# Optimization experiments

Hardware: AMD Instinct MI355X
Metric: run time of the kernel (lower is better)

Reference implementation:

```python
import jax, jax.numpy as jnp
import numpy as np

NUM_SEG = 533  # ~ 400*400/300 superpixels from SLIC
C_FEAT = 2112
H = W = 400
SIM_THRESH = 0.97


def setup_inputs() -> dict:
    key = jax.random.key(0)
    ks = jax.random.split(key, 8)
    inp = {
        "feature_maps": jax.random.normal(ks[0], (C_FEAT, H, W), jnp.float32),
        "sp": jax.random.randint(ks[1], (H, W), 0, NUM_SEG, jnp.int32),
        "y": jax.random.randint(ks[2], (H, W), 0, 3, jnp.int32),
        "w1": jax.random.normal(ks[3], (C_FEAT, 1024), jnp.float32) * 0.02,
        "b1": jnp.zeros((1024,), jnp.float32),
        "w2": jax.random.normal(ks[4], (1024, 1024), jnp.float32) * 0.02,
        "b2": jnp.zeros((1024,), jnp.float32),
        "w3": jax.random.normal(ks[5], (1024, 32), jnp.float32) * 0.02,
        "b3": jnp.zeros((32,), jnp.float32),
        "wc": jax.random.normal(ks[6], (32, 2), jnp.float32) * 0.02,
        "bc": jnp.zeros((2,), jnp.float32),
    }
    return inp


def reference(feature_maps, sp, y, w1, b1, w2, b2, w3, b3, wc, bc):
    C = feature_maps.shape[0]
    feats = feature_maps.reshape(C, -1).T            # [HW, C]
    seg = sp.reshape(-1)                             # [HW]

    # fused per-superpixel gather + mean (replaces the per-segment Python loop)
    sums = jax.ops.segment_sum(feats, seg, num_segments=NUM_SEG)          # [S, C]
    cnts = jax.ops.segment_sum(jnp.ones_like(seg, dtype=feats.dtype), seg,
                               num_segments=NUM_SEG)                      # [S]
    mean_feat = sums / jnp.maximum(cnts, 1.0)[:, None]                    # [S, C]

    # per-superpixel majority label over classes {0,1,2}
    onehot = jax.nn.one_hot(y.reshape(-1), 3, dtype=jnp.float32)          # [HW, 3]
    counts = jax.ops.segment_sum(onehot, seg, num_segments=NUM_SEG)       # [S, 3]
    lab = jnp.argmax(counts, axis=1)                                      # first max, like torch
    ones_c, twos_c = counts[:, 1], counts[:, 2]
    tie_break = jnp.where(twos_c > ones_c, 2, jnp.where(ones_c > twos_c, 1, 0))
    lab = jnp.where(lab == 0, tie_break, lab)                             # [S]

    # batched MLP + classifier (replaces per-segment calls)
    h = jax.nn.relu(mean_feat @ w1 + b1)
    h = jax.nn.relu(h @ w2 + b2)
    h = jax.nn.relu(h @ w3 + b3)
    preds = jax.nn.softmax(h @ wc + bc, axis=-1)                          # [S, 2]

    # cosine-similarity kNN label propagation (matmul form of the O(n*m) loop)
    labeled = lab != 0
    det = jax.lax.stop_gradient(mean_feat)
    nrm = det / jnp.maximum(jnp.linalg.norm(det, axis=1, keepdims=True), 1e-12)
    aff = nrm @ nrm.T                                                     # [S, S]
    aff_masked = jnp.where(labeled[None, :], aff, -jnp.inf)               # cols: labeled only
    best = jnp.max(aff_masked, axis=1)
    best_idx = jnp.argmax(aff_masked, axis=1)
    propagate = (~labeled) & (best >= SIM_THRESH)
    new_lab = jnp.where(propagate, lab[best_idx], lab)                    # [S]

    return preds, lab, labeled, new_lab
```

## Files before the change

kernel.cpp:

```cpp
#include <hip/hip_runtime.h>
#include <math.h>

#define NSEG 533
#define CFEAT 2112
#define PIX 160000
#define SIM_THRESH 0.97f
#define RPG 1250
#define NCG 33
#define RTOT (RPG * NCG)
#define NBLK 256

typedef __attribute__((ext_vector_type(4))) float f32x4;
typedef __attribute__((ext_vector_type(4))) int   i32x4;
typedef __attribute__((ext_vector_type(8))) short bf16x8;

__device__ inline unsigned short f2bf_u16(float f) {
    unsigned u = __builtin_bit_cast(unsigned, f);
    return (unsigned short)((u + 0x7FFFu + ((u >> 16) & 1u)) >> 16);
}
__device__ inline unsigned pkbf(float a, float b) {
    unsigned r;
    asm("v_cvt_pk_bf16_f32 %0, %1, %2" : "=v"(r) : "v"(a), "v"(b));
    return r;
}

__global__ __launch_bounds__(256) void k_counts(const int* __restrict__ sp,
                                                const int* __restrict__ y,
                                                int* __restrict__ c3) {
    int p = blockIdx.x * 256 + threadIdx.x;
    if (p < PIX) atomicAdd(&c3[sp[p] * 3 + y[p]], 1);
}

__global__ __launch_bounds__(256) void k_labels(const int* __restrict__ c3,
                                                int* __restrict__ lab,
                                                float* __restrict__ invc,
                                                float* __restrict__ out) {
    int s = blockIdx.x * 256 + threadIdx.x;
    if (s >= NSEG) return;
    int c0 = c3[s * 3 + 0], c1 = c3[s * 3 + 1], c2 = c3[s * 3 + 2];
    int cnt = c0 + c1 + c2;
    int idx = 0, best = c0;
    if (c1 > best) { best = c1; idx = 1; }
    if (c2 > best) { best = c2; idx = 2; }
    if (idx == 0) idx = (c2 > c1) ? 2 : ((c1 > c2) ? 1 : 0);
    lab[s] = idx;
    invc[s] = 1.0f / (float)(cnt > 0 ? cnt : 1);
    out[1066 + s] = (float)idx;
    out[1599 + s] = (idx != 0) ? 1.0f : 0.0f;
}

__global__ __launch_bounds__(1024, 4) void k_segsum_mfma(const float* __restrict__ fm,
                                                         const int* __restrict__ sp,
                                                         float* __restrict__ sums) {
    __shared__ char Bs[2][64 * 256];
    const int tid = threadIdx.x;
    const int lane = tid & 63, wave = tid >> 6;
    const int r = lane & 15, kg = lane >> 4;
    const int nmt = (wave < 2) ? 3 : 2;
    const int rswz = (r & 7) << 4;
    const int sch = tid >> 4;
    const int spx = tid & 15;
    const int wswz = (sch & 7) << 4;

    long long t0 = ((long long)blockIdx.x * RTOT) / NBLK;
    const long long t1 = ((long long)(blockIdx.x + 1) * RTOT) / NBLK;

    while (t0 < t1) {
        const int cg = (int)(t0 / RPG);
        const int r0 = (int)(t0 - (long long)cg * RPG);
        const long long cgend = (long long)(cg + 1) * RPG;
        const int rend = (int)(((t1 < cgend) ? t1 : cgend) - (long long)cg * RPG);
        const int c0 = cg * 64;
        const float* fmg = fm + (size_t)(c0 + sch) * PIX;

        f32x4 acc[3][4] = {};

        {
            const float* src = fmg + r0 * 128 + spx * 8;
            f32x4 u0 = *(const f32x4*)src;
            f32x4 u1 = *(const f32x4*)(src + 4);
            uint4 w = { pkbf(u0[0], u0[1]), pkbf(u0[2], u0[3]),
                        pkbf(u1[0], u1[1]), pkbf(u1[2], u1[3]) };
            *(uint4*)(Bs[r0 & 1] + sch * 256 + ((spx * 16) ^ wswz)) = w;
        }
        __syncthreads();

        for (int rr = r0; rr < rend; ++rr) {
            const bool pf = (rr + 1 < rend);
            f32x4 u0 = {}, u1 = {};
            if (pf) {
                const float* src = fmg + (rr + 1) * 128 + spx * 8;
                u0 = *(const f32x4*)src;
                u1 = *(const f32x4*)(src + 4);
            }
            const char* bufc = Bs[rr & 1];
            const int* spr = sp + rr * 128 + kg * 8;
            i32x4 sa = *(const i32x4*)spr;
            i32x4 sb = *(const i32x4*)(spr + 4);

            #pragma unroll
            for (int ks = 0; ks < 4; ++ks) {
                i32x4 na, nb;
                if (ks < 3) {
                    na = *(const i32x4*)(spr + (ks + 1) * 32);
                    nb = *(const i32x4*)(spr + (ks + 1) * 32 + 4);
                }
                bf16x8 vb[4];
                #pragma unroll
                for (int nt = 0; nt < 4; ++nt) {
                    vb[nt] = *(const bf16x8*)(bufc + (nt * 16 + r) * 256 +
                                              ((ks * 64 + kg * 16) ^ rswz));
                }
                int seg[8] = { sa[0], sa[1], sa[2], sa[3], sb[0], sb[1], sb[2], sb[3] };
                #pragma unroll
                for (int i = 0; i < 3; ++i) {
                    if (i < nmt) {
                        const int tm = (i < 2) ? wave * 2 + i : 32 + wave;
                        const int tgt = tm * 16 + r;
                        unsigned w0 = ((seg[0] == tgt) ? 0x00003F80u : 0u) |
                                      ((seg[1] == tgt) ? 0x3F800000u : 0u);
                        unsigned w1 = ((seg[2] == tgt) ? 0x00003F80u : 0u) |
                                      ((seg[3] == tgt) ? 0x3F800000u : 0u);
                        unsigned w2 = ((seg[4] == tgt) ? 0x00003F80u : 0u) |
                                      ((seg[5] == tgt) ? 0x3F800000u : 0u);
                        unsigned w3 = ((seg[6] == tgt) ? 0x00003F80u : 0u) |
                                      ((seg[7] == tgt) ? 0x3F800000u : 0u);
                        uint4 w4 = { w0, w1, w2, w3 };
                        bf16x8 va = __builtin_bit_cast(bf16x8, w4);
                        acc[i][0] = __builtin_amdgcn_mfma_f32_16x16x32_bf16(va, vb[0], acc[i][0], 0, 0, 0);
                        acc[i][1] = __builtin_amdgcn_mfma_f32_16x16x32_bf16(va, vb[1], acc[i][1], 0, 0, 0);
                        acc[i][2] = __builtin_amdgcn_mfma_f32_16x16x32_bf16(va, vb[2], acc[i][2], 0, 0, 0);
                        acc[i][3] = __builtin_amdgcn_mfma_f32_16x16x32_bf16(va, vb[3], acc[i][3], 0, 0, 0);
                    }
                }
                if (ks < 3) { sa = na; sb = nb; }
            }

            if (pf) {
                uint4 w = { pkbf(u0[0], u0[1]), pkbf(u0[2], u0[3]),
                            pkbf(u1[0], u1[1]), pkbf(u1[2], u1[3]) };
                *(uint4*)(Bs[(rr + 1) & 1] + sch * 256 + ((spx * 16) ^ wswz)) = w;
            }
            __syncthreads();
        }

        #pragma unroll
        for (int i = 0; i < 3; ++i) {
            if (i < nmt) {
                const int tm = (i < 2) ? wave * 2 + i : 32 + wave;
                #pragma unroll
                for (int nt = 0; nt < 4; ++nt) {
                    #pragma unroll
                    for (int q = 0; q < 4; ++q) {
                        int s = tm * 16 + kg * 4 + q;
                        unsafeAtomicAdd(&sums[(size_t)s * CFEAT + c0 + nt * 16 + r],
                                        acc[i][nt][q]);
                    }
                }
            }
        }
        t0 = (t1 < cgend) ? t1 : cgend;
        if (t0 < t1) __syncthreads();
    }
}

__global__ __launch_bounds__(256) void k_mean(float* __restrict__ feat,
                                              unsigned short* __restrict__ featbf,
                                              const float* __restrict__ invc,
                                              float* __restrict__ invn) {
    int s = blockIdx.x;
    float ic = invc[s];
    float ss = 0.0f;
    for (int c = threadIdx.x; c < CFEAT; c += 256) {
        float v = feat[(size_t)s * CFEAT + c] * ic;
        feat[(size_t)s * CFEAT + c] = v;
        featbf[(size_t)s * CFEAT + c] = f2bf_u16(v);
        ss += v * v;
    }
    __shared__ float red[256];
    red[threadIdx.x] = ss;
    __syncthreads();
    for (int st = 128; st > 0; st >>= 1) {
        if (threadIdx.x < st) red[threadIdx.x] += red[threadIdx.x + st];
        __syncthreads();
    }
    if (threadIdx.x == 0) invn[s] = 1.0f / fmaxf(sqrtf(red[0]), 1e-12f);
}

__global__ __launch_bounds__(256) void k_cvtT(const float* __restrict__ in,
                                              unsigned short* __restrict__ outT,
                                              int K, int N) {
    __shared__ float s[32][33];
    int n0 = blockIdx.x * 32, k0 = blockIdx.y * 32;
    int lx = threadIdx.x & 31, ly = threadIdx.x >> 5;
    #pragma unroll
    for (int p = 0; p < 4; ++p)
        s[ly + p * 8][lx] = in[(size_t)(k0 + ly + p * 8) * N + n0 + lx];
    __syncthreads();
    #pragma unroll
    for (int p = 0; p < 4; ++p)
        outT[(size_t)(n0 + ly + p * 8) * K + k0 + lx] = f2bf_u16(s[lx][ly + p * 8]);
}

template <int RELU>
__global__ __launch_bounds__(256) void gemm_bf16(const unsigned short* __restrict__ A,
                                                 const unsigned short* __restrict__ Bt,
                                                 const float* __restrict__ bias,
                                                 float* __restrict__ Cf,
                                                 unsigned short* __restrict__ Cb,
                                                 int M, int N, int K) {
    __shared__ char As[64 * 128];
    __shared__ char Bs[64 * 128];
    const int tid = threadIdx.x;
    const int lane = tid & 63, wave = tid >> 6;
    const int r = lane & 15, kg = lane >> 4;
    const int m0 = blockIdx.y * 64, n0 = blockIdx.x * 64;
    const int row = tid >> 2, colw = tid & 3;
    const int swz = (row & 7) << 4;
    f32x4 acc[4] = {};

    for (int k0 = 0; k0 < K; k0 += 64) {
        {
            uint4 v0 = {}, v1 = {};
            if (m0 + row < M) {
                const unsigned short* src = A + (size_t)(m0 + row) * K + k0 + colw * 16;
                v0 = *(const uint4*)src;
                v1 = *(const uint4*)(src + 8);
            }
            *(uint4*)(As + row * 128 + ((colw * 32) ^ swz)) = v0;
            *(uint4*)(As + row * 128 + ((colw * 32 + 16) ^ swz)) = v1;
        }
        {
            uint4 v0 = {}, v1 = {};
            if (n0 + row < N) {
                const unsigned short* src = Bt + (size_t)(n0 + row) * K + k0 + colw * 16;
                v0 = *(const uint4*)src;
                v1 = *(const uint4*)(src + 8);
            }
            *(uint4*)(Bs + row * 128 + ((colw * 32) ^ swz)) = v0;
            *(uint4*)(Bs + row * 128 + ((colw * 32 + 16) ^ swz)) = v1;
        }
        __syncthreads();
        #pragma unroll
        for (int ks = 0; ks < 2; ++ks) {
            const int arow = wave * 16 + r;
            bf16x8 va = *(const bf16x8*)(As + arow * 128 + (((ks * 64) + kg * 16) ^ ((arow & 7) << 4)));
            #pragma unroll
            for (int nt = 0; nt < 4; ++nt) {
                const int brow = nt * 16 + r;
                bf16x8 vb = *(const bf16x8*)(Bs + brow * 128 + (((ks * 64) + kg * 16) ^ ((brow & 7) << 4)));
                acc[nt] = __builtin_amdgcn_mfma_f32_16x16x32_bf16(va, vb, acc[nt], 0, 0, 0);
            }
        }
        __syncthreads();
    }

    #pragma unroll
    for (int nt = 0; nt < 4; ++nt) {
        #pragma unroll
        for (int q = 0; q < 4; ++q) {
            int gr = m0 + wave * 16 + kg * 4 + q;
            int gc = n0 + nt * 16 + r;
            if (gr < M && gc < N) {
                float v = acc[nt][q];
                if (bias) v += bias[gc];
                if (RELU) v = fmaxf(v, 0.0f);
                if (Cf) Cf[(size_t)gr * N + gc] = v;
                if (Cb) Cb[(size_t)gr * N + gc] = f2bf_u16(v);
            }
        }
    }
}

__global__ __launch_bounds__(256) void k_prop(const float* __restrict__ aff,
                                              const int* __restrict__ lab,
                                              const float* __restrict__ invn,
                                              float* __restrict__ out) {
    int i = blockIdx.x;
    float invi = invn[i];
    float best = -INFINITY;
    int bidx = 0;
    for (int j = threadIdx.x; j < NSEG; j += 256) {
        if (lab[j] != 0) {
            float v = aff[(size_t)i * NSEG + j] * invi * invn[j];
            if (v > best) { best = v; bidx = j; }
        }
    }
    __shared__ float bv[256];
    __shared__ int bi[256];
    bv[threadIdx.x] = best;
    bi[threadIdx.x] = bidx;
    __syncthreads();
    for (int st = 128; st > 0; st >>= 1) {
        if (threadIdx.x < st) {
            float v2 = bv[threadIdx.x + st];
            int i2 = bi[threadIdx.x + st];
            if (v2 > bv[threadIdx.x] ||
                (v2 == bv[threadIdx.x] && i2 < bi[threadIdx.x])) {
                bv[threadIdx.x] = v2;
                bi[threadIdx.x] = i2;
            }
        }
        __syncthreads();
    }
    if (threadIdx.x == 0) {
        int li = lab[i];
        int nl = li;
        if (li == 0 && bv[0] >= SIM_THRESH) nl = lab[bi[0]];
        out[2132 + i] = (float)nl;
    }
}

__global__ __launch_bounds__(256) void k_head(const float* __restrict__ h3,
                                              const float* __restrict__ wc,
                                              const float* __restrict__ bc,
                                              float* __restrict__ out) {
    int s = blockIdx.x * 256 + threadIdx.x;
    if (s >= NSEG) return;
    float z0 = bc[0], z1 = bc[1];
    #pragma unroll
    for (int k = 0; k < 32; k++) {
        float h = h3[s * 32 + k];
        z0 += h * wc[k * 2 + 0];
        z1 += h * wc[k * 2 + 1];
    }
    float m = fmaxf(z0, z1);
    float e0 = expf(z0 - m), e1 = expf(z1 - m);
    float inv = 1.0f / (e0 + e1);
    out[s * 2 + 0] = e0 * inv;
    out[s * 2 + 1] = e1 * inv;
}

extern "C" void kernel_launch(void* const* d_in, const int* in_sizes, int n_in,
                              void* d_out, int out_size, void* d_ws, size_t ws_size,
                              hipStream_t stream) {
    const float* fm = (const float*)d_in[0];
    const int* sp   = (const int*)d_in[1];
    const int* y    = (const int*)d_in[2];
    const float* w1 = (const float*)d_in[3];
    const float* b1 = (const float*)d_in[4];
    const float* w2 = (const float*)d_in[5];
    const float* b2 = (const float*)d_in[6];
    const float* w3 = (const float*)d_in[7];
    const float* b3 = (const float*)d_in[8];
    const float* wc = (const float*)d_in[9];
    const float* bc = (const float*)d_in[10];
    float* out = (float*)d_out;
    char* ws = (char*)d_ws;

    size_t off = 0;
    auto alloc = [&](size_t bytes) {
        size_t o = off;
        off += (bytes + 255) & ~(size_t)255;
        return o;
    };
    float*          feat   = (float*)(ws + alloc((size_t)544 * CFEAT * 4));
    unsigned short* featbf = (unsigned short*)(ws + alloc((size_t)544 * CFEAT * 2));
    unsigned short* w1T    = (unsigned short*)(ws + alloc((size_t)1024 * CFEAT * 2));
    unsigned short* w2T    = (unsigned short*)(ws + alloc((size_t)1024 * 1024 * 2));
    unsigned short* w3T    = (unsigned short*)(ws + alloc((size_t)32 * 1024 * 2));
    unsigned short* h1bf   = (unsigned short*)(ws + alloc((size_t)544 * 1024 * 2));
    unsigned short* h2bf   = (unsigned short*)(ws + alloc((size_t)544 * 1024 * 2));
    float*          h3     = (float*)(ws + alloc((size_t)544 * 32 * 4));
    float*          aff    = (float*)(ws + alloc((size_t)NSEG * NSEG * 4));
    int*            c3     = (int*)(ws + alloc((size_t)NSEG * 3 * 4));
    int*            lab    = (int*)(ws + alloc((size_t)NSEG * 4));
    float*          invc   = (float*)(ws + alloc((size_t)NSEG * 4));
    float*          invn   = (float*)(ws + alloc((size_t)NSEG * 4));

    hipMemsetAsync(feat, 0, (size_t)544 * CFEAT * 4, stream);
    hipMemsetAsync(c3, 0, (size_t)NSEG * 3 * 4, stream);

    k_cvtT<<<dim3(1024 / 32, CFEAT / 32), 256, 0, stream>>>(w1, w1T, CFEAT, 1024);
    k_cvtT<<<dim3(1024 / 32, 1024 / 32), 256, 0, stream>>>(w2, w2T, 1024, 1024);
    k_cvtT<<<dim3(32 / 32, 1024 / 32), 256, 0, stream>>>(w3, w3T, 1024, 32);

    k_counts<<<(PIX + 255) / 256, 256, 0, stream>>>(sp, y, c3);
    k_labels<<<3, 256, 0, stream>>>(c3, lab, invc, out);
    k_segsum_mfma<<<NBLK, 1024, 0, stream>>>(fm, sp, feat);
    k_mean<<<NSEG, 256, 0, stream>>>(feat, featbf, invc, invn);

    gemm_bf16<1><<<dim3(16, 9), 256, 0, stream>>>(featbf, w1T, b1, nullptr, h1bf, NSEG, 1024, CFEAT);
    gemm_bf16<1><<<dim3(16, 9), 256, 0, stream>>>(h1bf, w2T, b2, nullptr, h2bf, NSEG, 1024, 1024);
    gemm_bf16<1><<<dim3(1, 9), 256, 0, stream>>>(h2bf, w3T, b3, h3, nullptr, NSEG, 32, 1024);
    gemm_bf16<0><<<dim3(9, 9), 256, 0, stream>>>(featbf, featbf, nullptr, aff, nullptr, NSEG, NSEG, CFEAT);

    k_head<<<3, 256, 0, stream>>>(h3, wc, bc, out);
    k_prop<<<NSEG, 256, 0, stream>>>(aff, lab, invn, out);
}
```

Baseline: 684.3 us.

## Re-tile segment-sum MFMA kernel to 512-thread blocks with 9x2 wave tiles

The segment-sum kernel moves from 1024-thread blocks to 512-thread blocks and doubles the grid from 256 to 512 blocks. Each wave now covers 8-9 segment tiles by 2 channel tiles instead of 2-3 by 4, so each wave builds the one-hot A fragments for more segments and reads only two B fragments from LDS. The intent is finer work splitting and more blocks per CU while keeping the staging bandwidth. In exchange there are more accumulator registers (18 f32x4) and more one-hot compare work per wave, which may lower occupancy.

```diff
diff --git a/kernel.cpp b/kernel.cpp
--- a/kernel.cpp
+++ b/kernel.cpp
@@ -8,7 +8,7 @@
 #define RPG 1250
 #define NCG 33
 #define RTOT (RPG * NCG)
-#define NBLK 256
+#define NBLK 512
 
 typedef __attribute__((ext_vector_type(4))) float f32x4;
 typedef __attribute__((ext_vector_type(4))) int   i32x4;
@@ -49,17 +49,19 @@
     out[1599 + s] = (idx != 0) ? 1.0f : 0.0f;
 }
 
-__global__ __launch_bounds__(1024, 4) void k_segsum_mfma(const float* __restrict__ fm,
-                                                         const int* __restrict__ sp,
-                                                         float* __restrict__ sums) {
+__global__ __launch_bounds__(512, 4) void k_segsum_mfma(const float* __restrict__ fm,
+                                                        const int* __restrict__ sp,
+                                                        float* __restrict__ sums) {
     __shared__ char Bs[2][64 * 256];
     const int tid = threadIdx.x;
     const int lane = tid & 63, wave = tid >> 6;
     const int r = lane & 15, kg = lane >> 4;
-    const int nmt = (wave < 2) ? 3 : 2;
+    const int mg = wave >> 1, half = wave & 1;
+    const int nmt = (mg < 2) ? 9 : 8;
+    const int mt0 = (mg < 2) ? mg * 9 : 18 + (mg - 2) * 8;
     const int rswz = (r & 7) << 4;
-    const int sch = tid >> 4;
-    const int spx = tid & 15;
+    const int sch = tid >> 3;
+    const int spx = tid & 7;
     const int wswz = (sch & 7) << 4;
 
     long long t0 = ((long long)blockIdx.x * RTOT) / NBLK;
@@ -73,25 +75,33 @@
         const int c0 = cg * 64;
         const float* fmg = fm + (size_t)(c0 + sch) * PIX;
 
-        f32x4 acc[3][4] = {};
+        f32x4 acc[9][2] = {};
 
         {
-            const float* src = fmg + r0 * 128 + spx * 8;
+            const float* src = fmg + r0 * 128 + spx * 16;
             f32x4 u0 = *(const f32x4*)src;
             f32x4 u1 = *(const f32x4*)(src + 4);
-            uint4 w = { pkbf(u0[0], u0[1]), pkbf(u0[2], u0[3]),
-                        pkbf(u1[0], u1[1]), pkbf(u1[2], u1[3]) };
-            *(uint4*)(Bs[r0 & 1] + sch * 256 + ((spx * 16) ^ wswz)) = w;
+            f32x4 u2 = *(const f32x4*)(src + 8);
+            f32x4 u3 = *(const f32x4*)(src + 12);
+            uint4 wA = { pkbf(u0[0], u0[1]), pkbf(u0[2], u0[3]),
+                         pkbf(u1[0], u1[1]), pkbf(u1[2], u1[3]) };
+            uint4 wB = { pkbf(u2[0], u2[1]), pkbf(u2[2], u2[3]),
+                         pkbf(u3[0], u3[1]), pkbf(u3[2], u3[3]) };
+            char* dst = Bs[r0 & 1] + sch * 256;
+            *(uint4*)(dst + ((spx * 32) ^ wswz)) = wA;
+            *(uint4*)(dst + ((spx * 32 + 16) ^ wswz)) = wB;
         }
         __syncthreads();
 
         for (int rr = r0; rr < rend; ++rr) {
             const bool pf = (rr + 1 < rend);
-            f32x4 u0 = {}, u1 = {};
+            f32x4 u0 = {}, u1 = {}, u2 = {}, u3 = {};
             if (pf) {
-                const float* src = fmg + (rr + 1) * 128 + spx * 8;
+                const float* src = fmg + (rr + 1) * 128 + spx * 16;
                 u0 = *(const f32x4*)src;
                 u1 = *(const f32x4*)(src + 4);
+                u2 = *(const f32x4*)(src + 8);
+                u3 = *(const f32x4*)(src + 12);
             }
             const char* bufc = Bs[rr & 1];
             const int* spr = sp + rr * 128 + kg * 8;
@@ -105,18 +115,18 @@
                     na = *(const i32x4*)(spr + (ks + 1) * 32);
                     nb = *(const i32x4*)(spr + (ks + 1) * 32 + 4);
                 }
-                bf16x8 vb[4];
+                bf16x8 vb[2];
                 #pragma unroll
-                for (int nt = 0; nt < 4; ++nt) {
-                    vb[nt] = *(const bf16x8*)(bufc + (nt * 16 + r) * 256 +
-                                              ((ks * 64 + kg * 16) ^ rswz));
+                for (int j = 0; j < 2; ++j) {
+                    const int row = (half * 2 + j) * 16 + r;
+                    vb[j] = *(const bf16x8*)(bufc + row * 256 +
+                                             ((ks * 64 + kg * 16) ^ rswz));
                 }
                 int seg[8] = { sa[0], sa[1], sa[2], sa[3], sb[0], sb[1], sb[2], sb[3] };
                 #pragma unroll
-                for (int i = 0; i < 3; ++i) {
+                for (int i = 0; i < 9; ++i) {
                     if (i < nmt) {
-                        const int tm = (i < 2) ? wave * 2 + i : 32 + wave;
-                        const int tgt = tm * 16 + r;
+                        const int tgt = (mt0 + i) * 16 + r;
                         unsigned w0 = ((seg[0] == tgt) ? 0x00003F80u : 0u) |
                                       ((seg[1] == tgt) ? 0x3F800000u : 0u);
                         unsigned w1 = ((seg[2] == tgt) ? 0x00003F80u : 0u) |
@@ -129,32 +139,33 @@
                         bf16x8 va = __builtin_bit_cast(bf16x8, w4);
                         acc[i][0] = __builtin_amdgcn_mfma_f32_16x16x32_bf16(va, vb[0], acc[i][0], 0, 0, 0);
                         acc[i][1] = __builtin_amdgcn_mfma_f32_16x16x32_bf16(va, vb[1], acc[i][1], 0, 0, 0);
-                        acc[i][2] = __builtin_amdgcn_mfma_f32_16x16x32_bf16(va, vb[2], acc[i][2], 0, 0, 0);
-                        acc[i][3] = __builtin_amdgcn_mfma_f32_16x16x32_bf16(va, vb[3], acc[i][3], 0, 0, 0);
                     }
                 }
                 if (ks < 3) { sa = na; sb = nb; }
             }
 
             if (pf) {
-                uint4 w = { pkbf(u0[0], u0[1]), pkbf(u0[2], u0[3]),
-                            pkbf(u1[0], u1[1]), pkbf(u1[2], u1[3]) };
-                *(uint4*)(Bs[(rr + 1) & 1] + sch * 256 + ((spx * 16) ^ wswz)) = w;
+                uint4 wA = { pkbf(u0[0], u0[1]), pkbf(u0[2], u0[3]),
+                             pkbf(u1[0], u1[1]), pkbf(u1[2], u1[3]) };
+                uint4 wB = { pkbf(u2[0], u2[1]), pkbf(u2[2], u2[3]),
+                             pkbf(u3[0], u3[1]), pkbf(u3[2], u3[3]) };
+                char* dst = Bs[(rr + 1) & 1] + sch * 256;
+                *(uint4*)(dst + ((spx * 32) ^ wswz)) = wA;
+                *(uint4*)(dst + ((spx * 32 + 16) ^ wswz)) = wB;
             }
             __syncthreads();
         }
 
         #pragma unroll
-        for (int i = 0; i < 3; ++i) {
+        for (int i = 0; i < 9; ++i) {
             if (i < nmt) {
-                const int tm = (i < 2) ? wave * 2 + i : 32 + wave;
                 #pragma unroll
-                for (int nt = 0; nt < 4; ++nt) {
+                for (int j = 0; j < 2; ++j) {
                     #pragma unroll
                     for (int q = 0; q < 4; ++q) {
-                        int s = tm * 16 + kg * 4 + q;
-                        unsafeAtomicAdd(&sums[(size_t)s * CFEAT + c0 + nt * 16 + r],
-                                        acc[i][nt][q]);
+                        int s = (mt0 + i) * 16 + kg * 4 + q;
+                        unsafeAtomicAdd(&sums[(size_t)s * CFEAT + c0 + (half * 2 + j) * 16 + r],
+                                        acc[i][j][q]);
                     }
                 }
             }
@@ -377,7 +388,7 @@
 
     k_counts<<<(PIX + 255) / 256, 256, 0, stream>>>(sp, y, c3);
     k_labels<<<3, 256, 0, stream>>>(c3, lab, invc, out);
-    k_segsum_mfma<<<NBLK, 1024, 0, stream>>>(fm, sp, feat);
+    k_segsum_mfma<<<NBLK, 512, 0, stream>>>(fm, sp, feat);
     k_mean<<<NSEG, 256, 0, stream>>>(feat, featbf, invc, invn);
 
     gemm_bf16<1><<<dim3(16, 9), 256, 0, stream>>>(featbf, w1T, b1, nullptr, h1bf, NSEG, 1024, CFEAT);
```

Result: slower. 968.9 us (+41.6%).

## Deepen segment-sum LDS pipeline to six buffers with two rows per barrier

Applied to the files above, without the earlier changes.

The segment-sum MFMA kernel moves from double buffering to a six-slot shared-memory ring. Rows are prefetched four and five steps ahead, and two rows are processed per __syncthreads. This puts more global loads in flight and halves the number of barriers, to hide HBM latency in a bandwidth-bound reduction. In exchange, LDS use grows from 32KB to 96KB per block, which may reduce occupancy, and register pressure rises from holding more prefetched values.

```diff
diff --git a/kernel.cpp b/kernel.cpp
--- a/kernel.cpp
+++ b/kernel.cpp
@@ -9,6 +9,7 @@
 #define NCG 33
 #define RTOT (RPG * NCG)
 #define NBLK 256
+#define NBUF 6
 
 typedef __attribute__((ext_vector_type(4))) float f32x4;
 typedef __attribute__((ext_vector_type(4))) int   i32x4;
@@ -52,7 +53,7 @@
 __global__ __launch_bounds__(1024, 4) void k_segsum_mfma(const float* __restrict__ fm,
                                                          const int* __restrict__ sp,
                                                          float* __restrict__ sums) {
-    __shared__ char Bs[2][64 * 256];
+    __shared__ char Bs[NBUF][64 * 256];
     const int tid = threadIdx.x;
     const int lane = tid & 63, wave = tid >> 6;
     const int r = lane & 15, kg = lane >> 4;
@@ -71,33 +72,24 @@
         const long long cgend = (long long)(cg + 1) * RPG;
         const int rend = (int)(((t1 < cgend) ? t1 : cgend) - (long long)cg * RPG);
         const int c0 = cg * 64;
-        const float* fmg = fm + (size_t)(c0 + sch) * PIX;
+        const float* fmg = fm + (size_t)(c0 + sch) * PIX + spx * 8;
 
         f32x4 acc[3][4] = {};
 
-        {
-            const float* src = fmg + r0 * 128 + spx * 8;
+        auto stageTo = [&](int rr, int bi) {
+            const float* src = fmg + rr * 128;
             f32x4 u0 = *(const f32x4*)src;
             f32x4 u1 = *(const f32x4*)(src + 4);
             uint4 w = { pkbf(u0[0], u0[1]), pkbf(u0[2], u0[3]),
                         pkbf(u1[0], u1[1]), pkbf(u1[2], u1[3]) };
-            *(uint4*)(Bs[r0 & 1] + sch * 256 + ((spx * 16) ^ wswz)) = w;
-        }
-        __syncthreads();
-
-        for (int rr = r0; rr < rend; ++rr) {
-            const bool pf = (rr + 1 < rend);
-            f32x4 u0 = {}, u1 = {};
-            if (pf) {
-                const float* src = fmg + (rr + 1) * 128 + spx * 8;
-                u0 = *(const f32x4*)src;
-                u1 = *(const f32x4*)(src + 4);
-            }
-            const char* bufc = Bs[rr & 1];
+            *(uint4*)(Bs[bi] + sch * 256 + ((spx * 16) ^ wswz)) = w;
+        };
+
+        auto compute = [&](int rr, int bi) {
+            const char* bufc = Bs[bi];
             const int* spr = sp + rr * 128 + kg * 8;
             i32x4 sa = *(const i32x4*)spr;
             i32x4 sb = *(const i32x4*)(spr + 4);
-
             #pragma unroll
             for (int ks = 0; ks < 4; ++ks) {
                 i32x4 na, nb;
@@ -107,10 +99,9 @@
                 }
                 bf16x8 vb[4];
                 #pragma unroll
-                for (int nt = 0; nt < 4; ++nt) {
+                for (int nt = 0; nt < 4; ++nt)
                     vb[nt] = *(const bf16x8*)(bufc + (nt * 16 + r) * 256 +
                                               ((ks * 64 + kg * 16) ^ rswz));
-                }
                 int seg[8] = { sa[0], sa[1], sa[2], sa[3], sb[0], sb[1], sb[2], sb[3] };
                 #pragma unroll
                 for (int i = 0; i < 3; ++i) {
@@ -135,12 +126,49 @@
                 }
                 if (ks < 3) { sa = na; sb = nb; }
             }
-
-            if (pf) {
-                uint4 w = { pkbf(u0[0], u0[1]), pkbf(u0[2], u0[3]),
-                            pkbf(u1[0], u1[1]), pkbf(u1[2], u1[3]) };
-                *(uint4*)(Bs[(rr + 1) & 1] + sch * 256 + ((spx * 16) ^ wswz)) = w;
-            }
+        };
+
+        const int b0i = r0 % NBUF;
+        const int n = rend - r0;
+        stageTo(r0, b0i);
+        if (n > 1) stageTo(r0 + 1, (b0i + 1) % NBUF);
+        if (n > 2) stageTo(r0 + 2, (b0i + 2) % NBUF);
+        if (n > 3) stageTo(r0 + 3, (b0i + 3) % NBUF);
+        __syncthreads();
+
+        int bi = b0i;
+        for (int rr = r0; rr < rend; rr += 2) {
+            const bool p4 = (rr + 4 < rend);
+            const bool p5 = (rr + 5 < rend);
+            f32x4 a0 = {}, a1 = {}, e0 = {}, e1 = {};
+            if (p4) {
+                const float* s4 = fmg + (rr + 4) * 128;
+                a0 = *(const f32x4*)s4;
+                a1 = *(const f32x4*)(s4 + 4);
+            }
+            compute(rr, bi);
+            if (p5) {
+                const float* s5 = fmg + (rr + 5) * 128;
+                e0 = *(const f32x4*)s5;
+                e1 = *(const f32x4*)(s5 + 4);
+            }
+            if (p4) {
+                int wb = bi + 4; if (wb >= NBUF) wb -= NBUF;
+                uint4 w = { pkbf(a0[0], a0[1]), pkbf(a0[2], a0[3]),
+                            pkbf(a1[0], a1[1]), pkbf(a1[2], a1[3]) };
+                *(uint4*)(Bs[wb] + sch * 256 + ((spx * 16) ^ wswz)) = w;
+            }
+            if (rr + 1 < rend) {
+                int cb = bi + 1; if (cb >= NBUF) cb -= NBUF;
+                compute(rr + 1, cb);
+            }
+            if (p5) {
+                int wb = bi + 5; if (wb >= NBUF) wb -= NBUF;
+                uint4 w = { pkbf(e0[0], e0[1]), pkbf(e0[2], e0[3]),
+                            pkbf(e1[0], e1[1]), pkbf(e1[2], e1[3]) };
+                *(uint4*)(Bs[wb] + sch * 256 + ((spx * 16) ^ wswz)) = w;
+            }
+            bi += 2; if (bi >= NBUF) bi -= NBUF;
             __syncthreads();
         }
 
```

Result: no change. 679.4 us (-0.7%).

## Widen segsum channel tile to 96 with 256-pixel rows; shared-memory histogram for counts

Applied to the files above, without the earlier changes.

The segment-sum MFMA kernel now processes 96 channels per group (22 groups) and 256 pixels per row step, split into two staged halves interleaved with compute. This reuses each one-hot A fragment across 6 N-tiles instead of 4 and halves the number of channel groups, which cuts the redundant segment-id loads and mask construction. The cost is a larger LDS footprint (96 KB double-buffered), more accumulator registers, and idle staging threads. Separately, k_counts now builds a per-block shared-memory histogram over 5000 pixels before flushing to global atomics, replacing one global atomic per pixel.

```diff
diff --git a/kernel.cpp b/kernel.cpp
--- a/kernel.cpp
+++ b/kernel.cpp
@@ -5,8 +5,8 @@
 #define CFEAT 2112
 #define PIX 160000
 #define SIM_THRESH 0.97f
-#define RPG 1250
-#define NCG 33
+#define RPG 625
+#define NCG 22
 #define RTOT (RPG * NCG)
 #define NBLK 256
 
@@ -27,8 +27,19 @@
 __global__ __launch_bounds__(256) void k_counts(const int* __restrict__ sp,
                                                 const int* __restrict__ y,
                                                 int* __restrict__ c3) {
-    int p = blockIdx.x * 256 + threadIdx.x;
-    if (p < PIX) atomicAdd(&c3[sp[p] * 3 + y[p]], 1);
+    __shared__ int h[NSEG * 3];
+    for (int e = threadIdx.x; e < NSEG * 3; e += 256) h[e] = 0;
+    __syncthreads();
+    const int base = blockIdx.x * 5000;
+    for (int p = threadIdx.x; p < 5000; p += 256) {
+        int idx = base + p;
+        atomicAdd(&h[sp[idx] * 3 + y[idx]], 1);
+    }
+    __syncthreads();
+    for (int e = threadIdx.x; e < NSEG * 3; e += 256) {
+        int v = h[e];
+        if (v) atomicAdd(&c3[e], v);
+    }
 }
 
 __global__ __launch_bounds__(256) void k_labels(const int* __restrict__ c3,
@@ -52,14 +63,15 @@
 __global__ __launch_bounds__(1024, 4) void k_segsum_mfma(const float* __restrict__ fm,
                                                          const int* __restrict__ sp,
                                                          float* __restrict__ sums) {
-    __shared__ char Bs[2][64 * 256];
+    __shared__ char Bs[2][96 * 512];
     const int tid = threadIdx.x;
     const int lane = tid & 63, wave = tid >> 6;
     const int r = lane & 15, kg = lane >> 4;
     const int nmt = (wave < 2) ? 3 : 2;
     const int rswz = (r & 7) << 4;
-    const int sch = tid >> 4;
-    const int spx = tid & 15;
+    const int sch = tid >> 3;
+    const int spx = tid & 7;
+    const bool stg = (sch < 96);
     const int wswz = (sch & 7) << 4;
 
     long long t0 = ((long long)blockIdx.x * RTOT) / NBLK;
@@ -70,48 +82,47 @@
         const int r0 = (int)(t0 - (long long)cg * RPG);
         const long long cgend = (long long)(cg + 1) * RPG;
         const int rend = (int)(((t1 < cgend) ? t1 : cgend) - (long long)cg * RPG);
-        const int c0 = cg * 64;
-        const float* fmg = fm + (size_t)(c0 + sch) * PIX;
-
-        f32x4 acc[3][4] = {};
-
-        {
-            const float* src = fmg + r0 * 128 + spx * 8;
+        const int c0 = cg * 96;
+        const float* fmg = stg ? (fm + (size_t)(c0 + sch) * PIX + spx * 16) : fm;
+
+        f32x4 acc[3][6] = {};
+
+        auto stageHalf = [&](int rr, int h) {
+            if (!stg) return;
+            const float* src = fmg + rr * 256 + h * 128;
             f32x4 u0 = *(const f32x4*)src;
             f32x4 u1 = *(const f32x4*)(src + 4);
-            uint4 w = { pkbf(u0[0], u0[1]), pkbf(u0[2], u0[3]),
-                        pkbf(u1[0], u1[1]), pkbf(u1[2], u1[3]) };
-            *(uint4*)(Bs[r0 & 1] + sch * 256 + ((spx * 16) ^ wswz)) = w;
-        }
-        __syncthreads();
-
-        for (int rr = r0; rr < rend; ++rr) {
-            const bool pf = (rr + 1 < rend);
-            f32x4 u0 = {}, u1 = {};
-            if (pf) {
-                const float* src = fmg + (rr + 1) * 128 + spx * 8;
-                u0 = *(const f32x4*)src;
-                u1 = *(const f32x4*)(src + 4);
-            }
+            f32x4 u2 = *(const f32x4*)(src + 8);
+            f32x4 u3 = *(const f32x4*)(src + 12);
+            uint4 wA = { pkbf(u0[0], u0[1]), pkbf(u0[2], u0[3]),
+                         pkbf(u1[0], u1[1]), pkbf(u1[2], u1[3]) };
+            uint4 wB = { pkbf(u2[0], u2[1]), pkbf(u2[2], u2[3]),
+                         pkbf(u3[0], u3[1]), pkbf(u3[2], u3[3]) };
+            char* dst = Bs[rr & 1] + sch * 512;
+            const int b0 = h * 256 + spx * 32;
+            *(uint4*)(dst + ((b0) ^ wswz)) = wA;
+            *(uint4*)(dst + ((b0 + 16) ^ wswz)) = wB;
+        };
+
+        auto computeHalf = [&](int rr, int ks0) {
             const char* bufc = Bs[rr & 1];
-            const int* spr = sp + rr * 128 + kg * 8;
+            const int* spr = sp + rr * 256 + ks0 * 32 + kg * 8;
             i32x4 sa = *(const i32x4*)spr;
             i32x4 sb = *(const i32x4*)(spr + 4);
-
             #pragma unroll
-            for (int ks = 0; ks < 4; ++ks) {
+            for (int k = 0; k < 4; ++k) {
+                const int ks = ks0 + k;
                 i32x4 na, nb;
-                if (ks < 3) {
-                    na = *(const i32x4*)(spr + (ks + 1) * 32);
-                    nb = *(const i32x4*)(spr + (ks + 1) * 32 + 4);
-                }
-                bf16x8 vb[4];
-                #pragma unroll
-                for (int nt = 0; nt < 4; ++nt) {
-                    vb[nt] = *(const bf16x8*)(bufc + (nt * 16 + r) * 256 +
-                                              ((ks * 64 + kg * 16) ^ rswz));
+                if (k < 3) {
+                    na = *(const i32x4*)(spr + (k + 1) * 32);
+                    nb = *(const i32x4*)(spr + (k + 1) * 32 + 4);
                 }
                 int seg[8] = { sa[0], sa[1], sa[2], sa[3], sb[0], sb[1], sb[2], sb[3] };
+                bf16x8 vb[6];
+                #pragma unroll
+                for (int nt = 0; nt < 6; ++nt)
+                    vb[nt] = *(const bf16x8*)(bufc + (nt * 16 + r) * 512 +
+                                              ((ks * 64 + kg * 16) ^ rswz));
                 #pragma unroll
                 for (int i = 0; i < 3; ++i) {
                     if (i < nmt) {
@@ -131,16 +142,24 @@
                         acc[i][1] = __builtin_amdgcn_mfma_f32_16x16x32_bf16(va, vb[1], acc[i][1], 0, 0, 0);
                         acc[i][2] = __builtin_amdgcn_mfma_f32_16x16x32_bf16(va, vb[2], acc[i][2], 0, 0, 0);
                         acc[i][3] = __builtin_amdgcn_mfma_f32_16x16x32_bf16(va, vb[3], acc[i][3], 0, 0, 0);
+                        acc[i][4] = __builtin_amdgcn_mfma_f32_16x16x32_bf16(va, vb[4], acc[i][4], 0, 0, 0);
+                        acc[i][5] = __builtin_amdgcn_mfma_f32_16x16x32_bf16(va, vb[5], acc[i][5], 0, 0, 0);
                     }
                 }
-                if (ks < 3) { sa = na; sb = nb; }
-            }
-
-            if (pf) {
-                uint4 w = { pkbf(u0[0], u0[1]), pkbf(u0[2], u0[3]),
-                            pkbf(u1[0], u1[1]), pkbf(u1[2], u1[3]) };
-                *(uint4*)(Bs[(rr + 1) & 1] + sch * 256 + ((spx * 16) ^ wswz)) = w;
-            }
+                if (k < 3) { sa = na; sb = nb; }
+            }
+        };
+
+        stageHalf(r0, 0);
+        stageHalf(r0, 1);
+        __syncthreads();
+
+        for (int rr = r0; rr < rend; ++rr) {
+            const bool pf = (rr + 1 < rend);
+            if (pf) stageHalf(rr + 1, 0);
+            computeHalf(rr, 0);
+            if (pf) stageHalf(rr + 1, 1);
+            computeHalf(rr, 4);
             __syncthreads();
         }
 
@@ -149,7 +168,7 @@
             if (i < nmt) {
                 const int tm = (i < 2) ? wave * 2 + i : 32 + wave;
                 #pragma unroll
-                for (int nt = 0; nt < 4; ++nt) {
+                for (int nt = 0; nt < 6; ++nt) {
                     #pragma unroll
                     for (int q = 0; q < 4; ++q) {
                         int s = tm * 16 + kg * 4 + q;
@@ -375,7 +394,7 @@
     k_cvtT<<<dim3(1024 / 32, 1024 / 32), 256, 0, stream>>>(w2, w2T, 1024, 1024);
     k_cvtT<<<dim3(32 / 32, 1024 / 32), 256, 0, stream>>>(w3, w3T, 1024, 32);
 
-    k_counts<<<(PIX + 255) / 256, 256, 0, stream>>>(sp, y, c3);
+    k_counts<<<32, 256, 0, stream>>>(sp, y, c3);
     k_labels<<<3, 256, 0, stream>>>(c3, lab, invc, out);
     k_segsum_mfma<<<NBLK, 1024, 0, stream>>>(fm, sp, feat);
     k_mean<<<NSEG, 256, 0, stream>>>(feat, featbf, invc, invn);
```

Result: slower. 969.6 us (+41.7%).
